# Kernel optimization log

Measured on AMD Instinct MI355X. Metric: run time of the kernel, lower is better.

The kernel has to match this reference:

```python
import jax, jax.numpy as jnp
import numpy as np

EPS = 1e-6
HID = 2048; N_HEADS = 16; Q_LORA = 768; KV_LORA = 512
ROPE_D = 64; NOPE_D = 128; V_D = 128
IDX_H = 32; IDX_D = 128; IDX_TOPK = 512
N_EXP = 8; TOPK = 4; N_GROUP = 4; TOPK_GROUP = 2
MOE_I = 512; SHARED_I = 512; ROUTED_SCALE = 2.5
T = 1024
NEG = -1e30


def _rms(x, w, eps=EPS):
    x = x.astype(jnp.float32)
    return x * jax.lax.rsqrt(jnp.mean(x * x, axis=-1, keepdims=True) + eps) * w


def _ln(x, w, b, eps=EPS):
    x = x.astype(jnp.float32)
    m = jnp.mean(x, axis=-1, keepdims=True)
    v = jnp.mean((x - m) ** 2, axis=-1, keepdims=True)
    return (x - m) * jax.lax.rsqrt(v + eps) * w + b


def _rope_cs(positions, dim):
    inv = 1.0 / (10000.0 ** (jnp.arange(0, dim, 2, dtype=jnp.float32) / dim))
    f = positions.astype(jnp.float32)[:, None] * inv[None, :]  # [T, dim/2]
    return jnp.cos(f), jnp.sin(f)


def _rope(x, cos, sin):
    # neox-style rotate-half over last dim
    d = x.shape[-1] // 2
    x1, x2 = x[..., :d], x[..., d:]
    while cos.ndim < x.ndim:
        cos, sin = cos[:, None], sin[:, None]
    return jnp.concatenate([x1 * cos - x2 * sin, x2 * cos + x1 * sin], axis=-1)


def setup_inputs() -> dict:
    key = jax.random.key(0)
    ks = iter(jax.random.split(key, 32))
    w = lambda *s: jax.random.normal(next(ks), s, jnp.float32) * 0.02
    inp = {
        'positions': jnp.arange(T, dtype=jnp.int32),
        'hidden_states': jax.random.normal(next(ks), (T, HID), jnp.float32),
        'residual': jax.random.normal(next(ks), (T, HID), jnp.float32),
        'w_input_ln': jnp.ones((HID,), jnp.float32),
        'w_post_ln': jnp.ones((HID,), jnp.float32),
        'w_step1': w(Q_LORA + KV_LORA + ROPE_D + IDX_D + IDX_H, HID),
        'w_q_a_ln': jnp.ones((Q_LORA,), jnp.float32),
        'w_kv_a_ln': jnp.ones((KV_LORA,), jnp.float32),
        'idx_k_ln_w': jnp.ones((IDX_D,), jnp.float32),
        'idx_k_ln_b': jnp.zeros((IDX_D,), jnp.float32),
        'w_step3': w(IDX_H * IDX_D + N_HEADS * (NOPE_D + ROPE_D), Q_LORA),
        'W_UK_T': w(N_HEADS, NOPE_D, KV_LORA),
        'W_UV': w(N_HEADS, KV_LORA, V_D),
        'w_o': w(HID, N_HEADS * V_D),
        'gate_w': w(N_EXP, HID),
        'gate_bias': jnp.zeros((N_EXP,), jnp.float32),
        'shared_gate_up': w(2 * SHARED_I, HID),
        'shared_down': w(HID, SHARED_I),
        'exp_gate_up': w(N_EXP, 2 * MOE_I, HID),
        'exp_down': w(N_EXP, HID, MOE_I),
    }
    return inp


def reference(positions, hidden_states, residual, w_input_ln, w_post_ln, w_step1,
              w_q_a_ln, w_kv_a_ln, idx_k_ln_w, idx_k_ln_b, w_step3, W_UK_T, W_UV,
              w_o, gate_w, gate_bias, shared_gate_up, shared_down, exp_gate_up, exp_down):
    Tn = hidden_states.shape[0]
    rows = jnp.arange(Tn)
    # (allreduce is identity at tp=1) + residual add + RMSNorm
    res = hidden_states.astype(jnp.float32) + residual.astype(jnp.float32)
    h = _rms(res, w_input_ln)
    # ---- Step 1: fused qkv_a + indexer_wk + indexer_weights_proj GEMM ----
    s1 = h @ w_step1.T
    o0 = 0
    q_c = s1[:, o0:o0 + Q_LORA]; o0 += Q_LORA
    kv_c = s1[:, o0:o0 + KV_LORA]; o0 += KV_LORA
    k_pe = s1[:, o0:o0 + ROPE_D]; o0 += ROPE_D
    idx_k = s1[:, o0:o0 + IDX_D]; o0 += IDX_D
    idx_w_raw = s1[:, o0:o0 + IDX_H]
    cos, sin = _rope_cs(positions, ROPE_D)
    # fused_norm_rope: norms + rope on k_pe / indexer-k
    q_c = _rms(q_c, w_q_a_ln)
    kv_c = _rms(kv_c, w_kv_a_ln)
    k_pe = _rope(k_pe, cos, sin)
    idx_k = _ln(idx_k, idx_k_ln_w, idx_k_ln_b)
    idx_k = jnp.concatenate([_rope(idx_k[:, :ROPE_D], cos, sin), idx_k[:, ROPE_D:]], axis=-1)
    # ---- Step 3: fused indexer_wq_b + q_b_proj GEMM ----
    s3 = q_c @ w_step3.T
    idx_q = s3[:, :IDX_H * IDX_D].reshape(Tn, IDX_H, IDX_D)
    q = s3[:, IDX_H * IDX_D:].reshape(Tn, N_HEADS, NOPE_D + ROPE_D)
    q_nope, q_pe = q[..., :NOPE_D], q[..., NOPE_D:]
    # absorb W_UK: [T,H,nope] x [H,nope,kv_lora] -> [T,H,kv_lora]
    ql_nope = jnp.einsum('thn,hnk->thk', q_nope, W_UK_T)
    q_pe = _rope(q_pe, cos, sin)
    idx_q = jnp.concatenate([_rope(idx_q[..., :ROPE_D], cos, sin), idx_q[..., ROPE_D:]], axis=-1)
    idx_q = idx_q * (IDX_D ** -0.5)            # indexer softmax scale
    idx_w = idx_w_raw * (IDX_H ** -0.5)        # per-head weights scale
    # ---- sparse attention indexer: relu(q.k) head-weighted sum, causal top-k ----
    il = jnp.einsum('thd,sd->ths', idx_q, idx_k)          # [T,Hi,S]
    iscores = jnp.einsum('ths,th->ts', jax.nn.relu(il), idx_w)
    causal = positions[:, None] >= positions[None, :]
    iscores = jnp.where(causal, iscores, NEG)
    topk_idx = jax.lax.top_k(iscores, IDX_TOPK)[1]        # [T, IDX_TOPK]
    tmask = jnp.zeros((Tn, Tn), bool).at[rows[:, None], topk_idx].set(True)
    mask = causal & tmask
    # ---- MLA MQA attention in latent space ----
    mqa_q = jnp.concatenate([ql_nope, jnp.broadcast_to(q_pe, (Tn, N_HEADS, ROPE_D))], axis=-1)
    kv = jnp.concatenate([kv_c, k_pe], axis=-1)           # [S, kv_lora+rope]
    att = jnp.einsum('thd,sd->hts', mqa_q, kv) * ((NOPE_D + ROPE_D) ** -0.5)
    att = jnp.where(mask[None], att, NEG)
    p = jax.nn.softmax(att, axis=-1)
    o = jnp.einsum('hts,sk->thk', p, kv_c)                # [T,H,kv_lora]
    o = jnp.einsum('thk,hkv->thv', o, W_UV).reshape(Tn, N_HEADS * V_D)
    attn_out = o @ w_o.T
    # add + RMSNorm
    res2 = attn_out + res
    h2 = _rms(res2, w_post_ln)
    # ---- MoE: DeepSeekV3 sigmoid grouped routing + shared experts ----
    glog = h2 @ gate_w.T
    sg = jax.nn.sigmoid(glog)
    sc = sg + gate_bias
    gsz = N_EXP // N_GROUP
    grp = sc.reshape(Tn, N_GROUP, gsz)
    grp_score = jax.lax.top_k(grp, min(2, gsz))[0].sum(-1)
    gidx = jax.lax.top_k(grp_score, TOPK_GROUP)[1]
    gmask = jnp.zeros((Tn, N_GROUP), bool).at[rows[:, None], gidx].set(True)
    emask = jnp.repeat(gmask, gsz, axis=1)
    sc_m = jnp.where(emask, sc, NEG)
    _, tid = jax.lax.top_k(sc_m, TOPK)
    tw = jnp.take_along_axis(sg, tid, axis=1)
    tw = tw / (tw.sum(-1, keepdims=True) + 1e-20) * ROUTED_SCALE
    comb = jnp.zeros((Tn, N_EXP), jnp.float32).at[rows[:, None], tid].set(tw)
    # routed experts (dense masked combine as reference for grouped-GEMM dispatch)
    gu = jnp.einsum('th,eih->tei', h2, exp_gate_up)       # [T,E,2I]
    act = jax.nn.silu(gu[..., :MOE_I]) * gu[..., MOE_I:]
    routed_e = jnp.einsum('tei,ehi->teh', act, exp_down)  # [T,E,H]
    routed = jnp.einsum('te,teh->th', comb, routed_e)
    # shared experts
    gus = h2 @ shared_gate_up.T
    shared = (jax.nn.silu(gus[:, :SHARED_I]) * gus[:, SHARED_I:]) @ shared_down.T
    out = shared + routed
    return out, res2
```

## Files before the change

kernel.cpp:

```cpp
#include <hip/hip_runtime.h>
#include <math.h>

static constexpr int TT  = 1024;
static constexpr int HID = 2048;
static constexpr int NH  = 16;
static constexpr int QL  = 768;
static constexpr int KVL = 512;
static constexpr int RD  = 64;
static constexpr int IH  = 32;
static constexpr int ID  = 128;
static constexpr int S1W = QL + KVL + RD + ID + IH;
static constexpr int S3W = IH*ID + NH*(128+RD);

#define SCALE_ATT 0.07216878364870323f
#define SC_IDXQ   0.08838834764831845f
#define SC_IDXW   0.17677669529663687f
#define NEGR      -1e30f
#define NEGL      -3.0e38f

typedef __bf16 bf16x8 __attribute__((ext_vector_type(8)));
typedef float  f32x4  __attribute__((ext_vector_type(4)));

#define GLD_LDS16(g, l) __builtin_amdgcn_global_load_lds( \
    (const __attribute__((address_space(1))) void*)(g),   \
    (__attribute__((address_space(3))) void*)(l), 16, 0, 0)

__device__ __forceinline__ void pipe_barrier() {
  __builtin_amdgcn_sched_barrier(0);
  asm volatile("" ::: "memory");
  __builtin_amdgcn_s_barrier();
  asm volatile("" ::: "memory");
  __builtin_amdgcn_sched_barrier(0);
}
__device__ __forceinline__ void wait_vm8() {
  asm volatile("s_waitcnt vmcnt(8)" ::: "memory");
  __builtin_amdgcn_sched_barrier(0);
}
__device__ __forceinline__ void wait_vm0() {
  asm volatile("s_waitcnt vmcnt(0)" ::: "memory");
  __builtin_amdgcn_sched_barrier(0);
}

__device__ __forceinline__ unsigned short f2b(float x) {
  union { float f; unsigned u; } v; v.f = x;
  unsigned r = v.u + 0x7FFFu + ((v.u >> 16) & 1u);
  return (unsigned short)(r >> 16);
}
__device__ __forceinline__ float b2f(unsigned short u) {
  union { unsigned u; float f; } v; v.u = ((unsigned)u) << 16;
  return v.f;
}

__device__ __forceinline__ float blk_sum256(float v, float* s) {
  #pragma unroll
  for (int o = 32; o > 0; o >>= 1) v += __shfl_down(v, o, 64);
  __syncthreads();
  if ((threadIdx.x & 63) == 0) s[threadIdx.x >> 6] = v;
  __syncthreads();
  return s[0] + s[1] + s[2] + s[3];
}

__global__ __launch_bounds__(256) void k_prelude(const float* __restrict__ hs,
                                                 const float* __restrict__ rsd,
                                                 const float* __restrict__ w,
                                                 float* __restrict__ res,
                                                 unsigned short* __restrict__ hb) {
  int t = blockIdx.x;
  __shared__ float scr[4];
  float vals[8]; float ss = 0.f;
  #pragma unroll
  for (int r = 0; r < 8; r++) {
    int d = threadIdx.x + 256*r;
    float v = hs[(size_t)t*HID + d] + rsd[(size_t)t*HID + d];
    vals[r] = v; res[(size_t)t*HID + d] = v; ss = fmaf(v, v, ss);
  }
  ss = blk_sum256(ss, scr);
  float inv = 1.f/sqrtf(ss/(float)HID + 1e-6f);
  #pragma unroll
  for (int r = 0; r < 8; r++) {
    int d = threadIdx.x + 256*r;
    hb[(size_t)t*HID + d] = f2b(vals[r]*inv*w[d]);
  }
}

__global__ __launch_bounds__(256) void k_res2(const float* __restrict__ attn1,
                                              const float* __restrict__ attn2,
                                              const float* __restrict__ res,
                                              const float* __restrict__ w,
                                              float* __restrict__ res2_out,
                                              float* __restrict__ h2,
                                              unsigned short* __restrict__ h2b) {
  int t = blockIdx.x;
  __shared__ float scr[4];
  float vals[8]; float ss = 0.f;
  #pragma unroll
  for (int r = 0; r < 8; r++) {
    int d = threadIdx.x + 256*r;
    float v = attn1[(size_t)t*HID + d] + attn2[(size_t)t*HID + d] + res[(size_t)t*HID + d];
    vals[r] = v; res2_out[(size_t)t*HID + d] = v; ss = fmaf(v, v, ss);
  }
  ss = blk_sum256(ss, scr);
  float inv = 1.f/sqrtf(ss/(float)HID + 1e-6f);
  #pragma unroll
  for (int r = 0; r < 8; r++) {
    int d = threadIdx.x + 256*r;
    float o = vals[r]*inv*w[d];
    h2[(size_t)t*HID + d] = o;
    h2b[(size_t)t*HID + d] = f2b(o);
  }
}

__global__ void k_ropecs(const int* __restrict__ pos, float* __restrict__ cosb, float* __restrict__ sinb) {
  int i = blockIdx.x*256 + threadIdx.x;
  if (i >= TT*32) return;
  int t = i >> 5, k = i & 31;
  double inv = pow(10000.0, -((double)(2*k))/64.0);
  double f = (double)pos[t] * inv;
  cosb[i] = (float)cos(f);
  sinb[i] = (float)sin(f);
}

__global__ void k_f2b(const float* __restrict__ s, unsigned short* __restrict__ d,
                      long long n, long long ntot) {
  long long stride = (long long)gridDim.x * 1024;
  for (long long i = ((long long)blockIdx.x*256 + threadIdx.x)*4; i < ntot; i += stride) {
    float x0, x1, x2, x3;
    if (i + 3 < n) { float4 v = *(const float4*)(s + i); x0=v.x; x1=v.y; x2=v.z; x3=v.w; }
    else {
      x0 = (i   < n) ? s[i]   : 0.f; x1 = (i+1 < n) ? s[i+1] : 0.f;
      x2 = (i+2 < n) ? s[i+2] : 0.f; x3 = (i+3 < n) ? s[i+3] : 0.f;
    }
    ushort4 o; o.x=f2b(x0); o.y=f2b(x1); o.z=f2b(x2); o.w=f2b(x3);
    *(ushort4*)(d + i) = o;
  }
}

__global__ void k_f2b4(const float* __restrict__ s0, unsigned short* __restrict__ d0, long long n0,
                       const float* __restrict__ s1, unsigned short* __restrict__ d1, long long n1,
                       const float* __restrict__ s2, unsigned short* __restrict__ d2, long long n2,
                       const float* __restrict__ s3, unsigned short* __restrict__ d3, long long n3) {
  long long ntot = n0 + n1 + n2 + n3;
  long long stride = (long long)gridDim.x * 1024;
  for (long long i = ((long long)blockIdx.x*256 + threadIdx.x)*4; i < ntot; i += stride) {
    const float* s; unsigned short* d; long long j = i;
    if (j < n0) { s = s0; d = d0; }
    else { j -= n0;
      if (j < n1) { s = s1; d = d1; }
      else { j -= n1;
        if (j < n2) { s = s2; d = d2; }
        else { j -= n2; s = s3; d = d3; } } }
    float4 v = *(const float4*)(s + j);
    ushort4 o; o.x=f2b(v.x); o.y=f2b(v.y); o.z=f2b(v.z); o.w=f2b(v.w);
    *(ushort4*)(d + j) = o;
  }
}

__global__ __launch_bounds__(256) void k_tconvb(const float* __restrict__ src,
                                                unsigned short* __restrict__ dst,
                                                int R, int C) {
  src += (size_t)blockIdx.z * R * C;
  dst += (size_t)blockIdx.z * R * C;
  __shared__ float tile[32][33];
  int c0 = blockIdx.x * 32, r0 = blockIdx.y * 32;
  int tx = threadIdx.x & 31, ty = threadIdx.x >> 5;
  #pragma unroll
  for (int i = 0; i < 4; i++) {
    int r = r0 + ty + i*8;
    tile[ty + i*8][tx] = src[(size_t)r*C + c0 + tx];
  }
  __syncthreads();
  #pragma unroll
  for (int i = 0; i < 4; i++) {
    int c = c0 + ty + i*8;
    dst[(size_t)c*R + r0 + tx] = f2b(tile[tx][ty + i*8]);
  }
}

template<int BM, int OUT, bool ILV, int MOE>
__global__ __launch_bounds__(256) void k_mgemm(
    const unsigned short* __restrict__ A, int lda, long long sA,
    const unsigned short* __restrict__ B, int ldb, long long sB,
    void* __restrict__ Cv, int ldc, long long sC,
    int N, int K, float alpha, int cskip, int ktri,
    int nseg, long long segA, long long segB,
    const float* __restrict__ comb,
    const int* __restrict__ cntp, const int* __restrict__ tokp) {
  constexpr int MR  = BM / 32;
  constexpr int ITA = BM / 32;
  const int row0 = blockIdx.y * BM;
  const int col0 = blockIdx.x * 128;
  const int tid  = threadIdx.x;
  if (cskip >= 0 && col0 > row0 + cskip) {
    if (OUT == 3) {
      float* C = (float*)Cv;
      for (int i = tid; i < BM*32; i += 256) {
        int rr = i >> 5, cc = (i & 31) * 4;
        float4 ng = make_float4(NEGR, NEGR, NEGR, NEGR);
        *(float4*)&C[(size_t)(row0 + rr)*ldc + col0 + cc] = ng;
      }
    }
    return;
  }
  const int zb = blockIdx.z;
  int cnt = 0; long long off = 0;
  if (MOE) {
    cnt = cntp[zb];
    for (int e = 0; e < zb; e++) off += cntp[e];
    if (row0 >= cnt) return;
  }
  __shared__ __align__(16) unsigned short As[2][BM*64];
  __shared__ __align__(16) unsigned short Bs[2][128*64];
  __shared__ float wlds[(OUT == 3) ? BM*32 : 1];
  const int wave = tid >> 6, lane = tid & 63;
  const int wm = wave >> 1, wn = wave & 1;
  A += (size_t)zb * (size_t)sA;
  B += (size_t)zb * (size_t)sB;
  if (MOE == 2) A += off * (long long)lda;

  if constexpr (OUT == 3) {
    for (int i = tid; i < BM*32; i += 256)
      wlds[i] = comb[(size_t)(row0 + (i >> 5))*32 + (i & 31)];
  }

  int tki[ITA];
  if (MOE == 1) {
    #pragma unroll
    for (int it = 0; it < ITA; it++) {
      int r = (wave*64 + it*256 + lane) >> 3;
      tki[it] = tokp[zb*1024 + row0 + r];
    }
  }

  f32x4 acc[MR][4] = {};
  f32x4 acc2[(OUT == 3) ? MR : 1][4] = {};
  const int l15 = lane & 15, l4 = lane >> 4;
  const int sx = l15 & 7;
  int Kend = K;
  if (ktri) {
    int kub = (((row0 + BM - 1) >> 7) + 1) << 7;
    if (kub < Kend) Kend = kub;
  }
  const int nk = Kend >> 6;
  const int nt = nseg * nk;

  auto STAGE = [&](int b, const unsigned short* Ab, const unsigned short* Bb, int k0) {
    #pragma unroll
    for (int it = 0; it < ITA; it++) {
      int base = wave*64 + it*256;
      int sidx = base + lane;
      int r = sidx >> 3, s = sidx & 7;
      int s_src = s ^ (r & 7);
      const unsigned short* ga;
      if (MOE == 1) ga = Ab + (size_t)tki[it]*lda + k0 + s_src*8;
      else          ga = Ab + (size_t)(row0 + r)*lda + k0 + s_src*8;
      GLD_LDS16(ga, &As[b][base*8]);
    }
    #pragma unroll
    for (int it = 0; it < 4; it++) {
      int base = wave*64 + it*256;
      int sidx = base + lane;
      int r = sidx >> 3, s = sidx & 7;
      int s_src = s ^ (r & 7);
      int rt = col0 + r;
      int srow = ILV ? ((rt >> 1) + (rt & 1)*512) : rt;
      const unsigned short* gb = Bb + (size_t)srow*ldb + k0 + s_src*8;
      GLD_LDS16(gb, &Bs[b][base*8]);
    }
  };

  STAGE(0, A, B, 0);
  int ks = 64, sg = 0;
  if (ks == Kend) { ks = 0; sg++; }
  if (nt > 1) {
    STAGE(1, A + (size_t)sg*segA, B + (size_t)sg*segB, ks);
    ks += 64; if (ks == Kend) { ks = 0; sg++; }
    wait_vm8();
  } else {
    wait_vm0();
  }
  pipe_barrier();

  for (int u = 0; u < nt; u++) {
    const int cur = u & 1;
    #pragma unroll
    for (int kc = 0; kc < 2; kc++) {
      const int sl = ((kc*4 + l4) ^ sx) << 3;
      bf16x8 fa[MR], fb[4];
      #pragma unroll
      for (int mf = 0; mf < MR; mf++)
        fa[mf] = *(const bf16x8*)&As[cur][(wm*(BM/2) + mf*16 + l15)*64 + sl];
      #pragma unroll
      for (int nf = 0; nf < 4; nf++)
        fb[nf] = *(const bf16x8*)&Bs[cur][(wn*64 + nf*16 + l15)*64 + sl];
      #pragma unroll
      for (int mf = 0; mf < MR; mf++)
        #pragma unroll
        for (int nf = 0; nf < 4; nf++)
          acc[mf][nf] = __builtin_amdgcn_mfma_f32_16x16x32_bf16(fa[mf], fb[nf], acc[mf][nf], 0, 0, 0);
    }
    if constexpr (OUT == 3) {
      if ((u + 1) % nk == 0) {
        int h = u / nk;
        #pragma unroll
        for (int mf = 0; mf < MR; mf++) {
          #pragma unroll
          for (int r = 0; r < 4; r++) {
            int rl = wm*(BM/2) + mf*16 + l4*4 + r;
            float w = wlds[rl*32 + h];
            #pragma unroll
            for (int nf = 0; nf < 4; nf++) {
              acc2[mf][nf][r] += fmaxf(acc[mf][nf][r], 0.f) * w;
              acc[mf][nf][r] = 0.f;
            }
          }
        }
      }
    }
    pipe_barrier();
    if (u + 1 < nt) {
      if (u + 2 < nt) {
        STAGE(cur, A + (size_t)sg*segA, B + (size_t)sg*segB, ks);
        ks += 64; if (ks == Kend) { ks = 0; sg++; }
        wait_vm8();
      } else {
        wait_vm0();
      }
      pipe_barrier();
    }
  }

  #pragma unroll
  for (int mf = 0; mf < MR; mf++) {
    #pragma unroll
    for (int nf = 0; nf < 4; nf++) {
      int n = col0 + wn*64 + nf*16 + l15;
      #pragma unroll
      for (int r = 0; r < 4; r++) {
        int m = row0 + wm*(BM/2) + mf*16 + l4*4 + r;
        if (OUT == 3) {
          float v = acc2[mf][nf][r];
          if (n > 512 + m) v = NEGR;
          ((float*)Cv)[(size_t)m*ldc + n] = v;
          continue;
        }
        float v = acc[mf][nf][r] * alpha;
        if (OUT == 2) {
          float p = __shfl_xor(v, 1, 64);
          if ((l15 & 1) == 0) {
            bool ok = true;
            long long mrow = m;
            float w;
            if (MOE == 1) {
              ok = (m < cnt); mrow = off + m;
              int tok = tokp[zb*1024 + m];
              w = (zb < 8) ? comb[tok*8 + zb] : 1.f;
            } else {
              w = (zb < 8) ? comb[m*8 + zb] : 1.f;
            }
            if (ok) {
              float rres = v/(1.f + expf(-v)) * p * w;
              ((unsigned short*)Cv)[(size_t)zb*sC + (size_t)mrow*ldc + (n >> 1)] = f2b(rres);
            }
          }
        } else if (n < N) {
          bool ok = true;
          long long mrow = m;
          if (MOE == 2) { ok = (m < cnt); mrow = off + m; }
          if (ok) {
            size_t idx = (size_t)mrow*ldc + n;
            if (OUT == 1) ((unsigned short*)Cv)[(size_t)zb*sC + idx] = f2b(v);
            else          ((float*)Cv)[(size_t)zb*sC + idx] = v;
          }
        }
      }
    }
  }
}

__global__ __launch_bounds__(256) void k_post1(const float* __restrict__ s1a,
    const float* __restrict__ s1b,
    const float* __restrict__ wq, const float* __restrict__ wkv,
    const float* __restrict__ lnw, const float* __restrict__ lnb,
    const float* __restrict__ cosb, const float* __restrict__ sinb,
    unsigned short* __restrict__ qcb, float* __restrict__ kvc,
    unsigned short* __restrict__ kvb, unsigned short* __restrict__ idxkb,
    float* __restrict__ idxw) {
  int t = blockIdx.x, tid = threadIdx.x;
  __shared__ float rowb[S1W];
  __shared__ float scr[4];
  __shared__ float yb[128];
  for (int d = tid; d < S1W; d += 256)
    rowb[d] = s1a[(size_t)t*S1W + d] + s1b[(size_t)t*S1W + d];
  __syncthreads();
  float ss = 0.f;
  for (int d = tid; d < QL; d += 256) { float v = rowb[d]; ss = fmaf(v,v,ss); }
  ss = blk_sum256(ss, scr);
  float inv = 1.f/sqrtf(ss/(float)QL + 1e-6f);
  for (int d = tid; d < QL; d += 256) qcb[(size_t)t*QL + d] = f2b(rowb[d]*inv*wq[d]);
  ss = 0.f;
  for (int d = tid; d < KVL; d += 256) { float v = rowb[QL+d]; ss = fmaf(v,v,ss); }
  ss = blk_sum256(ss, scr);
  inv = 1.f/sqrtf(ss/(float)KVL + 1e-6f);
  for (int d = tid; d < KVL; d += 256) {
    float v = rowb[QL+d]*inv*wkv[d];
    kvc[(size_t)t*KVL + d] = v;
    kvb[(size_t)t*576 + d] = f2b(v);
  }
  float sm = (tid < 128) ? rowb[1344 + tid] : 0.f;
  float tot = blk_sum256(sm, scr);
  float mean = tot / 128.f;
  float vs = 0.f;
  if (tid < 128) { float v = rowb[1344+tid] - mean; vs = v*v; }
  vs = blk_sum256(vs, scr);
  float ivn = 1.f/sqrtf(vs/128.f + 1e-6f);
  if (tid < 128) yb[tid] = (rowb[1344+tid]-mean)*ivn*lnw[tid] + lnb[tid];
  __syncthreads();
  if (tid < 32) {
    float c = cosb[t*32 + tid], s = sinb[t*32 + tid];
    idxkb[(size_t)t*ID + tid]      = f2b(yb[tid]*c - yb[32+tid]*s);
    idxkb[(size_t)t*ID + 32 + tid] = f2b(yb[32+tid]*c + yb[tid]*s);
    float x1 = rowb[1280+tid], x2 = rowb[1312+tid];
    kvb[(size_t)t*576 + 512 + tid] = f2b(x1*c - x2*s);
    kvb[(size_t)t*576 + 544 + tid] = f2b(x2*c + x1*s);
    idxw[(size_t)t*IH + tid] = rowb[1472+tid] * SC_IDXW;
  } else if (tid >= 64 && tid < 128) {
    idxkb[(size_t)t*ID + tid] = f2b(yb[tid]);
  }
}

__global__ __launch_bounds__(256) void k_post3b(const float* __restrict__ s3,
                                                const float* __restrict__ cosb,
                                                const float* __restrict__ sinb,
                                                unsigned short* __restrict__ s3b,
                                                unsigned short* __restrict__ qm) {
  int t = blockIdx.x, tid = threadIdx.x;
  const float* row = s3 + (size_t)t*S3W;
  __shared__ float buf[S3W];
  __shared__ float cs[32], sn[32];
  if (tid < 32) { cs[tid] = cosb[t*32+tid]; sn[tid] = sinb[t*32+tid]; }
  for (int d = tid; d < S3W; d += 256) buf[d] = row[d];
  __syncthreads();
  for (int p = tid; p < 1024; p += 256) {
    int h = p >> 5, d = p & 31;
    float c = cs[d], s = sn[d];
    float x1 = buf[h*ID + d], x2 = buf[h*ID + 32 + d];
    buf[h*ID + d]      = (x1*c - x2*s) * SC_IDXQ;
    buf[h*ID + 32 + d] = (x2*c + x1*s) * SC_IDXQ;
  }
  for (int p = tid; p < 2048; p += 256) {
    int h = p >> 6, d = 64 + (p & 63);
    buf[h*ID + d] *= SC_IDXQ;
  }
  for (int p = tid; p < 512; p += 256) {
    int h = p >> 5, d = p & 31;
    float c = cs[d], s = sn[d];
    int base = IH*ID + h*192 + 128;
    float x1 = buf[base + d], x2 = buf[base + 32 + d];
    float r1 = x1*c - x2*s, r2 = x2*c + x1*s;
    buf[base + d]      = r1;
    buf[base + 32 + d] = r2;
    qm[(size_t)t*9216 + h*576 + 512 + d]      = f2b(r1 * SCALE_ATT);
    qm[(size_t)t*9216 + h*576 + 544 + d]      = f2b(r2 * SCALE_ATT);
  }
  __syncthreads();
  unsigned short* orow = s3b + (size_t)t*S3W;
  for (int g = tid*4; g < S3W; g += 1024) {
    ushort4 o;
    o.x = f2b(buf[g]); o.y = f2b(buf[g+1]); o.z = f2b(buf[g+2]); o.w = f2b(buf[g+3]);
    *(ushort4*)(orow + g) = o;
  }
}

__global__ __launch_bounds__(512) void k_topk(const float* __restrict__ isc,
                                              unsigned char* __restrict__ mask) {
  int t = 512 + blockIdx.x;
  const float* row = isc + (size_t)blockIdx.x * TT;
  __shared__ unsigned long long keys[1024];
  int tid = threadIdx.x;
  for (int i = tid; i < 1024; i += 512) {
    float v = row[i];
    unsigned int b = __float_as_uint(v);
    unsigned int u = (b & 0x80000000u) ? ~b : (b | 0x80000000u);
    keys[i] = ((unsigned long long)u << 32) | (unsigned int)(1023 - i);
  }
  __syncthreads();
  for (int k = 2; k <= 1024; k <<= 1) {
    for (int j = k >> 1; j > 0; j >>= 1) {
      int i = ((tid & ~(j - 1)) << 1) | (tid & (j - 1));
      int l = i | j;
      unsigned long long a = keys[i], b = keys[l];
      bool up = ((i & k) == 0);
      if ((a < b) == up) { keys[i] = b; keys[l] = a; }
      __syncthreads();
    }
  }
  unsigned char* mrow = mask + (size_t)t * TT;
  for (int p = tid; p < 1024; p += 512) {
    int s = 1023 - (int)(keys[p] & 0xFFFFFFFFu);
    mrow[s] = (p < 512) ? (unsigned char)1 : (unsigned char)0;
  }
}

__global__ __launch_bounds__(256) void k_psoft(unsigned short* __restrict__ pb,
                                               const unsigned char* __restrict__ mask) {
  int b = blockIdx.x;
  int t = b & 1023, h = b >> 10;
  unsigned short* row = pb + ((size_t)h << 20) + ((size_t)t << 10);
  int tid = threadIdx.x;
  __shared__ float scr[4];
  int s0 = tid * 4;
  int rub = ((t >> 7) + 1) << 7;
  bool act = (s0 < rub);
  float v0 = 0.f, v1 = 0.f, v2 = 0.f, v3 = 0.f;
  bool m0 = false, m1 = false, m2 = false, m3 = false;
  if (act) {
    ushort4 raw = *(const ushort4*)(row + s0);
    v0 = b2f(raw.x); v1 = b2f(raw.y); v2 = b2f(raw.z); v3 = b2f(raw.w);
    if (t < 512) {
      m0 = (s0 <= t); m1 = (s0+1 <= t); m2 = (s0+2 <= t); m3 = (s0+3 <= t);
    } else {
      uchar4 mk = *(const uchar4*)(mask + (size_t)t*TT + s0);
      m0 = (s0 <= t) && mk.x; m1 = (s0+1 <= t) && mk.y;
      m2 = (s0+2 <= t) && mk.z; m3 = (s0+3 <= t) && mk.w;
    }
  }
  float mx = NEGL;
  if (m0) mx = v0;
  if (m1) mx = fmaxf(mx, v1);
  if (m2) mx = fmaxf(mx, v2);
  if (m3) mx = fmaxf(mx, v3);
  #pragma unroll
  for (int o = 32; o > 0; o >>= 1) mx = fmaxf(mx, __shfl_down(mx, o, 64));
  __syncthreads();
  if ((tid & 63) == 0) scr[tid >> 6] = mx;
  __syncthreads();
  mx = fmaxf(fmaxf(scr[0], scr[1]), fmaxf(scr[2], scr[3]));
  float p0 = m0 ? expf(v0 - mx) : 0.f;
  float p1 = m1 ? expf(v1 - mx) : 0.f;
  float p2 = m2 ? expf(v2 - mx) : 0.f;
  float p3 = m3 ? expf(v3 - mx) : 0.f;
  float sum = blk_sum256((p0+p1)+(p2+p3), scr);
  float inv = 1.f / sum;
  if (act) {
    ushort4 o;
    o.x = f2b(p0*inv); o.y = f2b(p1*inv); o.z = f2b(p2*inv); o.w = f2b(p3*inv);
    *(ushort4*)(row + s0) = o;
  }
}

__global__ __launch_bounds__(256) void k_gate(const float* __restrict__ h2,
                                              const float* __restrict__ gw,
                                              const float* __restrict__ gb,
                                              float* __restrict__ comb) {
  int t = blockIdx.x, tid = threadIdx.x;
  int e = tid >> 5, lane = tid & 31;
  __shared__ float gl[8];
  float p = 0.f;
  for (int d = lane; d < HID; d += 32) p = fmaf(h2[(size_t)t*HID+d], gw[(size_t)e*HID+d], p);
  #pragma unroll
  for (int o = 16; o > 0; o >>= 1) p += __shfl_down(p, o, 32);
  if (lane == 0) gl[e] = p;
  __syncthreads();
  if (tid == 0) {
    float sg[8], sc[8];
    #pragma unroll
    for (int i = 0; i < 8; i++) { sg[i] = 1.f/(1.f+expf(-gl[i])); sc[i] = sg[i] + gb[i]; }
    float gs[4];
    #pragma unroll
    for (int g = 0; g < 4; g++) gs[g] = sc[2*g] + sc[2*g+1];
    int g0 = 0;
    for (int g = 1; g < 4; g++) if (gs[g] > gs[g0]) g0 = g;
    int g1 = -1;
    for (int g = 0; g < 4; g++) { if (g == g0) continue; if (g1 < 0 || gs[g] > gs[g1]) g1 = g; }
    float wsum = 1e-20f;
    #pragma unroll
    for (int i = 0; i < 8; i++) { int g = i >> 1; if (g == g0 || g == g1) wsum += sg[i]; }
    #pragma unroll
    for (int i = 0; i < 8; i++) { int g = i >> 1; comb[t*8+i] = (g == g0 || g == g1) ? sg[i]/wsum*2.5f : 0.f; }
  }
}

__global__ __launch_bounds__(1024) void k_route(const float* __restrict__ comb,
                                                int* __restrict__ tokidx,
                                                int* __restrict__ rank,
                                                int* __restrict__ cntp) {
  int e = blockIdx.x;
  int t = threadIdx.x;
  if (e == 8) {
    tokidx[8*1024 + t] = t;
    if (t == 0) cntp[8] = 1024;
    return;
  }
  int lane = t & 63, w = t >> 6;
  bool sel = comb[t*8 + e] != 0.0f;
  unsigned long long bal = __ballot(sel);
  int pw = __popcll(bal & ((1ull << lane) - 1ull));
  int wt = __popcll(bal);
  __shared__ int wsum[16];
  if (lane == 0) wsum[w] = wt;
  __syncthreads();
  int woff = 0, total = 0;
  #pragma unroll
  for (int i = 0; i < 16; i++) { int v = wsum[i]; if (i < w) woff += v; total += v; }
  int pos = woff + pw;
  rank[t*8 + e] = sel ? pos : -1;
  if (sel) tokidx[e*1024 + pos] = t;
  __syncthreads();
  if (t >= total) tokidx[e*1024 + t] = 0;
  if (t == 0) cntp[e] = total;
}

__global__ __launch_bounds__(256) void k_rsum(const unsigned short* __restrict__ dpc,
                                              const int* __restrict__ rank,
                                              const int* __restrict__ cntp,
                                              float* __restrict__ out) {
  int t = blockIdx.x;
  int d = threadIdx.x * 8;
  int offs[8]; int acc_off = 0;
  #pragma unroll
  for (int e = 0; e < 8; e++) { offs[e] = acc_off; acc_off += cntp[e]; }
  const unsigned short* ps = dpc + (size_t)(acc_off + t)*2048 + d;
  ushort4 u0 = *(const ushort4*)ps;
  ushort4 u1 = *(const ushort4*)(ps + 4);
  float a[8];
  a[0]=b2f(u0.x); a[1]=b2f(u0.y); a[2]=b2f(u0.z); a[3]=b2f(u0.w);
  a[4]=b2f(u1.x); a[5]=b2f(u1.y); a[6]=b2f(u1.z); a[7]=b2f(u1.w);
  #pragma unroll
  for (int e = 0; e < 8; e++) {
    int r = rank[t*8 + e];
    if (r >= 0) {
      const unsigned short* p = dpc + (size_t)(offs[e] + r)*2048 + d;
      ushort4 b0 = *(const ushort4*)p;
      ushort4 b1 = *(const ushort4*)(p + 4);
      a[0]+=b2f(b0.x); a[1]+=b2f(b0.y); a[2]+=b2f(b0.z); a[3]+=b2f(b0.w);
      a[4]+=b2f(b1.x); a[5]+=b2f(b1.y); a[6]+=b2f(b1.z); a[7]+=b2f(b1.w);
    }
  }
  float* po = out + (size_t)t*2048 + d;
  *(float4*)po       = make_float4(a[0], a[1], a[2], a[3]);
  *(float4*)(po + 4) = make_float4(a[4], a[5], a[6], a[7]);
}

extern "C" void kernel_launch(void* const* d_in, const int* in_sizes, int n_in,
                              void* d_out, int out_size, void* d_ws, size_t ws_size,
                              hipStream_t stream) {
  const int*   positions = (const int*)d_in[0];
  const float* hs     = (const float*)d_in[1];
  const float* rsd    = (const float*)d_in[2];
  const float* w_in   = (const float*)d_in[3];
  const float* w_post = (const float*)d_in[4];
  const float* w_s1   = (const float*)d_in[5];
  const float* w_qln  = (const float*)d_in[6];
  const float* w_kvln = (const float*)d_in[7];
  const float* iklnw  = (const float*)d_in[8];
  const float* iklnb  = (const float*)d_in[9];
  const float* w_s3   = (const float*)d_in[10];
  const float* wukt   = (const float*)d_in[11];
  const float* wuv    = (const float*)d_in[12];
  const float* w_o    = (const float*)d_in[13];
  const float* gate_w = (const float*)d_in[14];
  const float* gate_b = (const float*)d_in[15];
  const float* sh_gu  = (const float*)d_in[16];
  const float* sh_dn  = (const float*)d_in[17];
  const float* ex_gu  = (const float*)d_in[18];
  const float* ex_dn  = (const float*)d_in[19];

  float* ws = (float*)d_ws;
  typedef unsigned short ush;
  float* RES   = ws + 0;
  float* COSB  = ws + 2097152;
  float* SINB  = ws + 2129920;
  float* KVC   = ws + 2162688;
  float* IDXW  = ws + 2883584;
  float* COMB  = ws + 2916352;
  ush*   HB    = (ush*)(ws + 2924544);
  ush*   WS1B  = (ush*)(ws + 3973120);
  float* S1P0  = ws + 5545984;
  ush*   QCB   = (ush*)(ws + 7086080);
  ush*   WS3B  = (ush*)(ws + 7479296);
  ush*   WOB   = (ush*)(ws + 7479296);
  float* S3    = ws + 10231808;
  float* S1P1  = ws + 10231808;
  ush*   S3B   = (ush*)(ws + 17571840);
  ush*   WUKTB = (ush*)(ws + 21241856);
  ush*   QMQAB = (ush*)(ws + 21766144);
  float* ISC   = ws + 26484736;
  unsigned char* MASK = (unsigned char*)(ws + 27009024);
  ush*   WUVB  = (ush*)(ws + 27271168);
  ush*   KVB   = (ush*)(ws + 27795456);
  ush*   VTB   = (ush*)(ws + 28090368);
  ush*   O2B   = (ush*)(ws + 28352512);
  ush*   IDXKB = (ush*)(ws + 31989760);
  ush*   PB    = (ush*)(ws + 10231808);
  ush*   OHB   = (ush*)(ws + 18620416);
  float* ATTNP = ws + 10231808;
  float* H2     = ws + 2924544;
  ush*   H2B    = (ush*)(ws + 5021696);
  ush*   EXGUB  = (ush*)(ws + 6070272);
  ush*   SHGUB  = (ush*)(ws + 14458880);
  ush*   EXDNB  = (ush*)(ws + 15507456);
  ush*   SHDNB  = (ush*)(ws + 19701760);
  ush*   ACTC   = (ush*)(ws + 20226048);
  ush*   DPC    = (ush*)(ws + 21536768);
  int*   TOKIDX = (int*)(ws + 32022528);
  int*   RANK   = (int*)(ws + 32031744);
  int*   CNT    = (int*)(ws + 32039936);

  float* OUT0 = (float*)d_out;
  float* OUT_RES2 = OUT0 + (size_t)TT*HID;

  k_prelude<<<TT, 256, 0, stream>>>(hs, rsd, w_in, RES, HB);
  k_ropecs<<<(TT*32)/256, 256, 0, stream>>>(positions, COSB, SINB);
  k_f2b<<<1024, 256, 0, stream>>>(w_s1, WS1B, 3080192LL, 3145728LL);
  k_f2b<<<1024, 256, 0, stream>>>(w_s3, WS3B, 5505024LL, 5505024LL);
  k_tconvb<<<dim3(16,4,16), 256, 0, stream>>>(wukt, WUKTB, 128, 512);
  k_tconvb<<<dim3(4,16,16), 256, 0, stream>>>(wuv, WUVB, 512, 128);
  k_mgemm<128,0,false,0><<<dim3(12,8,2), 256, 0, stream>>>(
      HB, 2048, 1024, WS1B, 2048, 1024, S1P0, S1W, 4685824,
      1504, 1024, 1.f, -1, 0, 1, 0, 0, nullptr, nullptr, nullptr);
  k_post1<<<TT, 256, 0, stream>>>(S1P0, S1P1, w_qln, w_kvln, iklnw, iklnb, COSB, SINB,
                                  QCB, KVC, KVB, IDXKB, IDXW);
  k_mgemm<128,0,false,0><<<dim3(56,8,1), 256, 0, stream>>>(
      QCB, 768, 0, WS3B, 768, 0, S3, S3W, 0,
      S3W, 768, 1.f, -1, 0, 1, 0, 0, nullptr, nullptr, nullptr);
  k_post3b<<<TT, 256, 0, stream>>>(S3, COSB, SINB, (ush*)S3B, QMQAB);
  k_f2b<<<1024, 256, 0, stream>>>(w_o, WOB, 4194304LL, 4194304LL);
  k_mgemm<128,1,false,0><<<dim3(4,8,16), 256, 0, stream>>>(
      S3B + 4096, S3W, 192, WUKTB, 128, 65536, QMQAB, 9216, 576,
      512, 128, SCALE_ATT, -1, 0, 1, 0, 0, nullptr, nullptr, nullptr);
  k_mgemm<64,3,false,0><<<dim3(8,8,1), 256, 0, stream>>>(
      S3B + (size_t)512*S3W, S3W, 0, IDXKB, 128, 0,
      ISC, 1024, 0, 1024, 128, 1.f, 575, 0, 32, 128, 0,
      IDXW + (size_t)512*IH, nullptr, nullptr);
  k_topk<<<512, 512, 0, stream>>>(ISC, MASK);
  k_tconvb<<<dim3(16,32,1), 256, 0, stream>>>(KVC, VTB, 1024, 512);
  k_mgemm<128,1,false,0><<<dim3(8,8,16), 256, 0, stream>>>(
      QMQAB, 9216, 576, KVB, 576, 0, PB, 1024, 1048576,
      1024, 576, 1.f, 127, 0, 1, 0, 0, nullptr, nullptr, nullptr);
  k_psoft<<<16384, 256, 0, stream>>>(PB, MASK);
  k_mgemm<128,1,false,0><<<dim3(4,8,16), 256, 0, stream>>>(
      PB, 1024, 1048576, VTB, 1024, 0, OHB, 512, 524288,
      512, 1024, 1.f, -1, 1, 1, 0, 0, nullptr, nullptr, nullptr);
  k_mgemm<128,1,false,0><<<dim3(1,8,16), 256, 0, stream>>>(
      OHB, 512, 524288, WUVB, 512, 65536, O2B, 2048, 128,
      128, 512, 1.f, -1, 0, 1, 0, 0, nullptr, nullptr, nullptr);
  k_mgemm<128,0,false,0><<<dim3(16,8,2), 256, 0, stream>>>(
      O2B, 2048, 1024, WOB, 2048, 1024, ATTNP, 2048, 2097152,
      2048, 1024, 1.f, -1, 0, 1, 0, 0, nullptr, nullptr, nullptr);
  k_res2<<<TT, 256, 0, stream>>>(ATTNP, ATTNP + 2097152, RES, w_post, OUT_RES2, H2, H2B);
  k_gate<<<TT, 256, 0, stream>>>(H2, gate_w, gate_b, COMB);
  k_route<<<9, 1024, 0, stream>>>(COMB, TOKIDX, RANK, CNT);
  k_f2b4<<<2048, 256, 0, stream>>>(ex_gu, EXGUB, 16777216LL,
                                   sh_gu, SHGUB, 2097152LL,
                                   ex_dn, EXDNB, 8388608LL,
                                   sh_dn, SHDNB, 1048576LL);
  k_mgemm<128,2,true,1><<<dim3(8,8,9), 256, 0, stream>>>(
      H2B, 2048, 0, EXGUB, 2048, 2097152, ACTC, 512, 0,
      1024, 2048, 1.f, -1, 0, 1, 0, 0, COMB, CNT, TOKIDX);
  k_mgemm<128,1,false,2><<<dim3(16,8,9), 256, 0, stream>>>(
      ACTC, 512, 0, EXDNB, 512, 1048576, DPC, 2048, 0,
      2048, 512, 1.f, -1, 0, 1, 0, 0, nullptr, CNT, nullptr);
  k_rsum<<<TT, 256, 0, stream>>>(DPC, RANK, CNT, OUT0);
}
```

Measured before the change: 459.5 us.

## Template GEMM K-tile depth, simplify pipeline, fuse rope/gate/weight-convert kernels

Adds a BK template parameter to the GEMM so most GEMMs stage 128-wide K tiles, which halves the number of barrier iterations but doubles LDS per block. The hand-tuned vmcnt-based double-buffer pipeline is replaced with a plain prefetch-next-then-compute loop that uses __syncthreads. Separately, the rope cos/sin table is folded into the prelude kernel, the MoE gate/routing is fused into the residual-norm kernel so the fp32 h2 buffer is never written, and the w_s3 and w_o bf16 conversions are merged into one launch. The goal is fewer launches and fewer K-loop barriers, at the risk of lower occupancy and less latency hiding.

```diff
diff --git a/kernel.cpp b/kernel.cpp
--- a/kernel.cpp
+++ b/kernel.cpp
@@ -25,22 +25,6 @@
     (const __attribute__((address_space(1))) void*)(g),   \
     (__attribute__((address_space(3))) void*)(l), 16, 0, 0)
 
-__device__ __forceinline__ void pipe_barrier() {
-  __builtin_amdgcn_sched_barrier(0);
-  asm volatile("" ::: "memory");
-  __builtin_amdgcn_s_barrier();
-  asm volatile("" ::: "memory");
-  __builtin_amdgcn_sched_barrier(0);
-}
-__device__ __forceinline__ void wait_vm8() {
-  asm volatile("s_waitcnt vmcnt(8)" ::: "memory");
-  __builtin_amdgcn_sched_barrier(0);
-}
-__device__ __forceinline__ void wait_vm0() {
-  asm volatile("s_waitcnt vmcnt(0)" ::: "memory");
-  __builtin_amdgcn_sched_barrier(0);
-}
-
 __device__ __forceinline__ unsigned short f2b(float x) {
   union { float f; unsigned u; } v; v.f = x;
   unsigned r = v.u + 0x7FFFu + ((v.u >> 16) & 1u);
@@ -63,10 +47,20 @@
 __global__ __launch_bounds__(256) void k_prelude(const float* __restrict__ hs,
                                                  const float* __restrict__ rsd,
                                                  const float* __restrict__ w,
+                                                 const int* __restrict__ pos,
                                                  float* __restrict__ res,
-                                                 unsigned short* __restrict__ hb) {
+                                                 unsigned short* __restrict__ hb,
+                                                 float* __restrict__ cosb,
+                                                 float* __restrict__ sinb) {
   int t = blockIdx.x;
   __shared__ float scr[4];
+  if (threadIdx.x < 32) {
+    int k = threadIdx.x;
+    double inv = pow(10000.0, -((double)(2*k))/64.0);
+    double f = (double)pos[t] * inv;
+    cosb[t*32 + k] = (float)cos(f);
+    sinb[t*32 + k] = (float)sin(f);
+  }
   float vals[8]; float ss = 0.f;
   #pragma unroll
   for (int r = 0; r < 8; r++) {
@@ -83,19 +77,23 @@
   }
 }
 
-__global__ __launch_bounds__(256) void k_res2(const float* __restrict__ attn1,
-                                              const float* __restrict__ attn2,
-                                              const float* __restrict__ res,
-                                              const float* __restrict__ w,
-                                              float* __restrict__ res2_out,
-                                              float* __restrict__ h2,
-                                              unsigned short* __restrict__ h2b) {
-  int t = blockIdx.x;
+__global__ __launch_bounds__(256) void k_res2g(const float* __restrict__ attn1,
+                                               const float* __restrict__ attn2,
+                                               const float* __restrict__ res,
+                                               const float* __restrict__ w,
+                                               const float* __restrict__ gw,
+                                               const float* __restrict__ gb,
+                                               float* __restrict__ res2_out,
+                                               unsigned short* __restrict__ h2b,
+                                               float* __restrict__ comb) {
+  int t = blockIdx.x, tid = threadIdx.x;
   __shared__ float scr[4];
+  __shared__ float h2l[HID];
+  __shared__ float gl[8];
   float vals[8]; float ss = 0.f;
   #pragma unroll
   for (int r = 0; r < 8; r++) {
-    int d = threadIdx.x + 256*r;
+    int d = tid + 256*r;
     float v = attn1[(size_t)t*HID + d] + attn2[(size_t)t*HID + d] + res[(size_t)t*HID + d];
     vals[r] = v; res2_out[(size_t)t*HID + d] = v; ss = fmaf(v, v, ss);
   }
@@ -103,21 +101,36 @@
   float inv = 1.f/sqrtf(ss/(float)HID + 1e-6f);
   #pragma unroll
   for (int r = 0; r < 8; r++) {
-    int d = threadIdx.x + 256*r;
+    int d = tid + 256*r;
     float o = vals[r]*inv*w[d];
-    h2[(size_t)t*HID + d] = o;
+    h2l[d] = o;
     h2b[(size_t)t*HID + d] = f2b(o);
   }
-}
-
-__global__ void k_ropecs(const int* __restrict__ pos, float* __restrict__ cosb, float* __restrict__ sinb) {
-  int i = blockIdx.x*256 + threadIdx.x;
-  if (i >= TT*32) return;
-  int t = i >> 5, k = i & 31;
-  double inv = pow(10000.0, -((double)(2*k))/64.0);
-  double f = (double)pos[t] * inv;
-  cosb[i] = (float)cos(f);
-  sinb[i] = (float)sin(f);
+  __syncthreads();
+  int e = tid >> 5, lane = tid & 31;
+  float p = 0.f;
+  for (int d = lane; d < HID; d += 32) p = fmaf(h2l[d], gw[(size_t)e*HID + d], p);
+  #pragma unroll
+  for (int o = 16; o > 0; o >>= 1) p += __shfl_down(p, o, 32);
+  if (lane == 0) gl[e] = p;
+  __syncthreads();
+  if (tid == 0) {
+    float sg[8], sc[8];
+    #pragma unroll
+    for (int i = 0; i < 8; i++) { sg[i] = 1.f/(1.f+expf(-gl[i])); sc[i] = sg[i] + gb[i]; }
+    float gs[4];
+    #pragma unroll
+    for (int g = 0; g < 4; g++) gs[g] = sc[2*g] + sc[2*g+1];
+    int g0 = 0;
+    for (int g = 1; g < 4; g++) if (gs[g] > gs[g0]) g0 = g;
+    int g1 = -1;
+    for (int g = 0; g < 4; g++) { if (g == g0) continue; if (g1 < 0 || gs[g] > gs[g1]) g1 = g; }
+    float wsum = 1e-20f;
+    #pragma unroll
+    for (int i = 0; i < 8; i++) { int g = i >> 1; if (g == g0 || g == g1) wsum += sg[i]; }
+    #pragma unroll
+    for (int i = 0; i < 8; i++) { int g = i >> 1; comb[t*8+i] = (g == g0 || g == g1) ? sg[i]/wsum*2.5f : 0.f; }
+  }
 }
 
 __global__ void k_f2b(const float* __restrict__ s, unsigned short* __restrict__ d,
@@ -176,7 +189,7 @@
   }
 }
 
-template<int BM, int OUT, bool ILV, int MOE>
+template<int BM, int BK, int OUT, bool ILV, int MOE>
 __global__ __launch_bounds__(256) void k_mgemm(
     const unsigned short* __restrict__ A, int lda, long long sA,
     const unsigned short* __restrict__ B, int ldb, long long sB,
@@ -185,8 +198,12 @@
     int nseg, long long segA, long long segB,
     const float* __restrict__ comb,
     const int* __restrict__ cntp, const int* __restrict__ tokp) {
-  constexpr int MR  = BM / 32;
-  constexpr int ITA = BM / 32;
+  constexpr int MR    = BM / 32;
+  constexpr int SLOTS = BK / 8;
+  constexpr int SH    = (BK == 64) ? 3 : 4;
+  constexpr int KC    = BK / 32;
+  constexpr int ITA   = BM * SLOTS / 256;
+  constexpr int ITB   = 128 * SLOTS / 256;
   const int row0 = blockIdx.y * BM;
   const int col0 = blockIdx.x * 128;
   const int tid  = threadIdx.x;
@@ -208,8 +225,8 @@
     for (int e = 0; e < zb; e++) off += cntp[e];
     if (row0 >= cnt) return;
   }
-  __shared__ __align__(16) unsigned short As[2][BM*64];
-  __shared__ __align__(16) unsigned short Bs[2][128*64];
+  __shared__ __align__(16) unsigned short As[2][BM*BK];
+  __shared__ __align__(16) unsigned short Bs[2][128*BK];
   __shared__ float wlds[(OUT == 3) ? BM*32 : 1];
   const int wave = tid >> 6, lane = tid & 63;
   const int wm = wave >> 1, wn = wave & 1;
@@ -226,7 +243,7 @@
   if (MOE == 1) {
     #pragma unroll
     for (int it = 0; it < ITA; it++) {
-      int r = (wave*64 + it*256 + lane) >> 3;
+      int r = (wave*64 + it*256 + lane) >> SH;
       tki[it] = tokp[zb*1024 + row0 + r];
     }
   }
@@ -240,7 +257,7 @@
     int kub = (((row0 + BM - 1) >> 7) + 1) << 7;
     if (kub < Kend) Kend = kub;
   }
-  const int nk = Kend >> 6;
+  const int nk = Kend / BK;
   const int nt = nseg * nk;
 
   auto STAGE = [&](int b, const unsigned short* Ab, const unsigned short* Bb, int k0) {
@@ -248,7 +265,7 @@
     for (int it = 0; it < ITA; it++) {
       int base = wave*64 + it*256;
       int sidx = base + lane;
-      int r = sidx >> 3, s = sidx & 7;
+      int r = sidx >> SH, s = sidx & (SLOTS - 1);
       int s_src = s ^ (r & 7);
       const unsigned short* ga;
       if (MOE == 1) ga = Ab + (size_t)tki[it]*lda + k0 + s_src*8;
@@ -256,10 +273,10 @@
       GLD_LDS16(ga, &As[b][base*8]);
     }
     #pragma unroll
-    for (int it = 0; it < 4; it++) {
+    for (int it = 0; it < ITB; it++) {
       int base = wave*64 + it*256;
       int sidx = base + lane;
-      int r = sidx >> 3, s = sidx & 7;
+      int r = sidx >> SH, s = sidx & (SLOTS - 1);
       int s_src = s ^ (r & 7);
       int rt = col0 + r;
       int srow = ILV ? ((rt >> 1) + (rt & 1)*512) : rt;
@@ -269,29 +286,27 @@
   };
 
   STAGE(0, A, B, 0);
-  int ks = 64, sg = 0;
-  if (ks == Kend) { ks = 0; sg++; }
-  if (nt > 1) {
-    STAGE(1, A + (size_t)sg*segA, B + (size_t)sg*segB, ks);
-    ks += 64; if (ks == Kend) { ks = 0; sg++; }
-    wait_vm8();
-  } else {
-    wait_vm0();
-  }
-  pipe_barrier();
+  int ks = BK, sg = 0;
+  if (ks == Kend) { ks = 0; sg = 1; }
+  __syncthreads();
+  int cur = 0;
 
   for (int u = 0; u < nt; u++) {
-    const int cur = u & 1;
-    #pragma unroll
-    for (int kc = 0; kc < 2; kc++) {
+    if (u + 1 < nt) {
+      STAGE(cur ^ 1, A + (size_t)sg*segA, B + (size_t)sg*segB, ks);
+      ks += BK;
+      if (ks == Kend) { ks = 0; sg++; }
+    }
+    #pragma unroll
+    for (int kc = 0; kc < KC; kc++) {
       const int sl = ((kc*4 + l4) ^ sx) << 3;
       bf16x8 fa[MR], fb[4];
       #pragma unroll
       for (int mf = 0; mf < MR; mf++)
-        fa[mf] = *(const bf16x8*)&As[cur][(wm*(BM/2) + mf*16 + l15)*64 + sl];
+        fa[mf] = *(const bf16x8*)&As[cur][(wm*(BM/2) + mf*16 + l15)*BK + sl];
       #pragma unroll
       for (int nf = 0; nf < 4; nf++)
-        fb[nf] = *(const bf16x8*)&Bs[cur][(wn*64 + nf*16 + l15)*64 + sl];
+        fb[nf] = *(const bf16x8*)&Bs[cur][(wn*64 + nf*16 + l15)*BK + sl];
       #pragma unroll
       for (int mf = 0; mf < MR; mf++)
         #pragma unroll
@@ -316,17 +331,8 @@
         }
       }
     }
-    pipe_barrier();
-    if (u + 1 < nt) {
-      if (u + 2 < nt) {
-        STAGE(cur, A + (size_t)sg*segA, B + (size_t)sg*segB, ks);
-        ks += 64; if (ks == Kend) { ks = 0; sg++; }
-        wait_vm8();
-      } else {
-        wait_vm0();
-      }
-      pipe_barrier();
-    }
+    __syncthreads();
+    cur ^= 1;
   }
 
   #pragma unroll
@@ -459,8 +465,8 @@
     float r1 = x1*c - x2*s, r2 = x2*c + x1*s;
     buf[base + d]      = r1;
     buf[base + 32 + d] = r2;
-    qm[(size_t)t*9216 + h*576 + 512 + d]      = f2b(r1 * SCALE_ATT);
-    qm[(size_t)t*9216 + h*576 + 544 + d]      = f2b(r2 * SCALE_ATT);
+    qm[(size_t)t*9216 + h*576 + 512 + d] = f2b(r1 * SCALE_ATT);
+    qm[(size_t)t*9216 + h*576 + 544 + d] = f2b(r2 * SCALE_ATT);
   }
   __syncthreads();
   unsigned short* orow = s3b + (size_t)t*S3W;
@@ -545,38 +551,6 @@
     ushort4 o;
     o.x = f2b(p0*inv); o.y = f2b(p1*inv); o.z = f2b(p2*inv); o.w = f2b(p3*inv);
     *(ushort4*)(row + s0) = o;
-  }
-}
-
-__global__ __launch_bounds__(256) void k_gate(const float* __restrict__ h2,
-                                              const float* __restrict__ gw,
-                                              const float* __restrict__ gb,
-                                              float* __restrict__ comb) {
-  int t = blockIdx.x, tid = threadIdx.x;
-  int e = tid >> 5, lane = tid & 31;
-  __shared__ float gl[8];
-  float p = 0.f;
-  for (int d = lane; d < HID; d += 32) p = fmaf(h2[(size_t)t*HID+d], gw[(size_t)e*HID+d], p);
-  #pragma unroll
-  for (int o = 16; o > 0; o >>= 1) p += __shfl_down(p, o, 32);
-  if (lane == 0) gl[e] = p;
-  __syncthreads();
-  if (tid == 0) {
-    float sg[8], sc[8];
-    #pragma unroll
-    for (int i = 0; i < 8; i++) { sg[i] = 1.f/(1.f+expf(-gl[i])); sc[i] = sg[i] + gb[i]; }
-    float gs[4];
-    #pragma unroll
-    for (int g = 0; g < 4; g++) gs[g] = sc[2*g] + sc[2*g+1];
-    int g0 = 0;
-    for (int g = 1; g < 4; g++) if (gs[g] > gs[g0]) g0 = g;
-    int g1 = -1;
-    for (int g = 0; g < 4; g++) { if (g == g0) continue; if (g1 < 0 || gs[g] > gs[g1]) g1 = g; }
-    float wsum = 1e-20f;
-    #pragma unroll
-    for (int i = 0; i < 8; i++) { int g = i >> 1; if (g == g0 || g == g1) wsum += sg[i]; }
-    #pragma unroll
-    for (int i = 0; i < 8; i++) { int g = i >> 1; comb[t*8+i] = (g == g0 || g == g1) ? sg[i]/wsum*2.5f : 0.f; }
   }
 }
 
@@ -678,7 +652,6 @@
   float* S1P0  = ws + 5545984;
   ush*   QCB   = (ush*)(ws + 7086080);
   ush*   WS3B  = (ush*)(ws + 7479296);
-  ush*   WOB   = (ush*)(ws + 7479296);
   float* S3    = ws + 10231808;
   float* S1P1  = ws + 10231808;
   ush*   S3B   = (ush*)(ws + 17571840);
@@ -691,10 +664,10 @@
   ush*   VTB   = (ush*)(ws + 28090368);
   ush*   O2B   = (ush*)(ws + 28352512);
   ush*   IDXKB = (ush*)(ws + 31989760);
+  ush*   WOB   = (ush*)(ws + 32055296);
   ush*   PB    = (ush*)(ws + 10231808);
   ush*   OHB   = (ush*)(ws + 18620416);
   float* ATTNP = ws + 10231808;
-  float* H2     = ws + 2924544;
   ush*   H2B    = (ush*)(ws + 5021696);
   ush*   EXGUB  = (ush*)(ws + 6070272);
   ush*   SHGUB  = (ush*)(ws + 14458880);
@@ -709,55 +682,56 @@
   float* OUT0 = (float*)d_out;
   float* OUT_RES2 = OUT0 + (size_t)TT*HID;
 
-  k_prelude<<<TT, 256, 0, stream>>>(hs, rsd, w_in, RES, HB);
-  k_ropecs<<<(TT*32)/256, 256, 0, stream>>>(positions, COSB, SINB);
+  k_prelude<<<TT, 256, 0, stream>>>(hs, rsd, w_in, positions, RES, HB, COSB, SINB);
   k_f2b<<<1024, 256, 0, stream>>>(w_s1, WS1B, 3080192LL, 3145728LL);
-  k_f2b<<<1024, 256, 0, stream>>>(w_s3, WS3B, 5505024LL, 5505024LL);
+  k_f2b4<<<2048, 256, 0, stream>>>(w_s3, WS3B, 5505024LL,
+                                   w_o,  WOB,  4194304LL,
+                                   w_s3, WS3B, 0LL,
+                                   w_s3, WS3B, 0LL);
   k_tconvb<<<dim3(16,4,16), 256, 0, stream>>>(wukt, WUKTB, 128, 512);
   k_tconvb<<<dim3(4,16,16), 256, 0, stream>>>(wuv, WUVB, 512, 128);
-  k_mgemm<128,0,false,0><<<dim3(12,8,2), 256, 0, stream>>>(
+  k_mgemm<128,128,0,false,0><<<dim3(12,8,2), 256, 0, stream>>>(
       HB, 2048, 1024, WS1B, 2048, 1024, S1P0, S1W, 4685824,
       1504, 1024, 1.f, -1, 0, 1, 0, 0, nullptr, nullptr, nullptr);
   k_post1<<<TT, 256, 0, stream>>>(S1P0, S1P1, w_qln, w_kvln, iklnw, iklnb, COSB, SINB,
                                   QCB, KVC, KVB, IDXKB, IDXW);
-  k_mgemm<128,0,false,0><<<dim3(56,8,1), 256, 0, stream>>>(
+  k_mgemm<128,128,0,false,0><<<dim3(56,8,1), 256, 0, stream>>>(
       QCB, 768, 0, WS3B, 768, 0, S3, S3W, 0,
       S3W, 768, 1.f, -1, 0, 1, 0, 0, nullptr, nullptr, nullptr);
   k_post3b<<<TT, 256, 0, stream>>>(S3, COSB, SINB, (ush*)S3B, QMQAB);
-  k_f2b<<<1024, 256, 0, stream>>>(w_o, WOB, 4194304LL, 4194304LL);
-  k_mgemm<128,1,false,0><<<dim3(4,8,16), 256, 0, stream>>>(
+  k_mgemm<128,64,1,false,0><<<dim3(4,8,16), 256, 0, stream>>>(
       S3B + 4096, S3W, 192, WUKTB, 128, 65536, QMQAB, 9216, 576,
       512, 128, SCALE_ATT, -1, 0, 1, 0, 0, nullptr, nullptr, nullptr);
-  k_mgemm<64,3,false,0><<<dim3(8,8,1), 256, 0, stream>>>(
+  k_mgemm<64,64,3,false,0><<<dim3(8,8,1), 256, 0, stream>>>(
       S3B + (size_t)512*S3W, S3W, 0, IDXKB, 128, 0,
       ISC, 1024, 0, 1024, 128, 1.f, 575, 0, 32, 128, 0,
       IDXW + (size_t)512*IH, nullptr, nullptr);
   k_topk<<<512, 512, 0, stream>>>(ISC, MASK);
   k_tconvb<<<dim3(16,32,1), 256, 0, stream>>>(KVC, VTB, 1024, 512);
-  k_mgemm<128,1,false,0><<<dim3(8,8,16), 256, 0, stream>>>(
+  k_mgemm<128,64,1,false,0><<<dim3(8,8,16), 256, 0, stream>>>(
       QMQAB, 9216, 576, KVB, 576, 0, PB, 1024, 1048576,
       1024, 576, 1.f, 127, 0, 1, 0, 0, nullptr, nullptr, nullptr);
   k_psoft<<<16384, 256, 0, stream>>>(PB, MASK);
-  k_mgemm<128,1,false,0><<<dim3(4,8,16), 256, 0, stream>>>(
+  k_mgemm<128,128,1,false,0><<<dim3(4,8,16), 256, 0, stream>>>(
       PB, 1024, 1048576, VTB, 1024, 0, OHB, 512, 524288,
       512, 1024, 1.f, -1, 1, 1, 0, 0, nullptr, nullptr, nullptr);
-  k_mgemm<128,1,false,0><<<dim3(1,8,16), 256, 0, stream>>>(
+  k_mgemm<128,128,1,false,0><<<dim3(1,8,16), 256, 0, stream>>>(
       OHB, 512, 524288, WUVB, 512, 65536, O2B, 2048, 128,
       128, 512, 1.f, -1, 0, 1, 0, 0, nullptr, nullptr, nullptr);
-  k_mgemm<128,0,false,0><<<dim3(16,8,2), 256, 0, stream>>>(
+  k_mgemm<128,128,0,false,0><<<dim3(16,8,2), 256, 0, stream>>>(
       O2B, 2048, 1024, WOB, 2048, 1024, ATTNP, 2048, 2097152,
       2048, 1024, 1.f, -1, 0, 1, 0, 0, nullptr, nullptr, nullptr);
-  k_res2<<<TT, 256, 0, stream>>>(ATTNP, ATTNP + 2097152, RES, w_post, OUT_RES2, H2, H2B);
-  k_gate<<<TT, 256, 0, stream>>>(H2, gate_w, gate_b, COMB);
+  k_res2g<<<TT, 256, 0, stream>>>(ATTNP, ATTNP + 2097152, RES, w_post, gate_w, gate_b,
+                                  OUT_RES2, H2B, COMB);
   k_route<<<9, 1024, 0, stream>>>(COMB, TOKIDX, RANK, CNT);
   k_f2b4<<<2048, 256, 0, stream>>>(ex_gu, EXGUB, 16777216LL,
                                    sh_gu, SHGUB, 2097152LL,
                                    ex_dn, EXDNB, 8388608LL,
                                    sh_dn, SHDNB, 1048576LL);
-  k_mgemm<128,2,true,1><<<dim3(8,8,9), 256, 0, stream>>>(
+  k_mgemm<128,128,2,true,1><<<dim3(8,8,9), 256, 0, stream>>>(
       H2B, 2048, 0, EXGUB, 2048, 2097152, ACTC, 512, 0,
       1024, 2048, 1.f, -1, 0, 1, 0, 0, COMB, CNT, TOKIDX);
-  k_mgemm<128,1,false,2><<<dim3(16,8,9), 256, 0, stream>>>(
+  k_mgemm<128,128,1,false,2><<<dim3(16,8,9), 256, 0, stream>>>(
       ACTC, 512, 0, EXDNB, 512, 1048576, DPC, 2048, 0,
       2048, 512, 1.f, -1, 0, 1, 0, 0, nullptr, CNT, nullptr);
   k_rsum<<<TT, 256, 0, stream>>>(DPC, RANK, CNT, OUT0);
```

Result: slower. 480.7 us (+4.6%).
